# Kernel optimization log

Hardware: AMD Instinct MI355X
Metric: run time of the kernel (lower is better)

## Reference

```python
import jax, jax.numpy as jnp
from jax import lax
import numpy as np

B, T, IN, H = 8192, 512, 5, 32


def setup_inputs() -> dict:
    key = jax.random.key(0)
    ks = jax.random.split(key, 7)
    s_ih = 1.0 / np.sqrt(H)
    return {
        "x": jax.random.normal(ks[0], (B, T, IN), dtype=jnp.float32),
        "W_ih": jax.random.normal(ks[1], (4 * H, IN), dtype=jnp.float32) * s_ih,
        "W_hh": jax.random.normal(ks[2], (4 * H, H), dtype=jnp.float32) * s_ih,
        "b_ih": jax.random.normal(ks[3], (4 * H,), dtype=jnp.float32) * s_ih,
        "b_hh": jax.random.normal(ks[4], (4 * H,), dtype=jnp.float32) * s_ih,
        "W_fc": jax.random.normal(ks[5], (1, H), dtype=jnp.float32) * s_ih,
        "b_fc": jax.random.normal(ks[6], (1,), dtype=jnp.float32) * s_ih,
    }


def reference(x, W_ih, W_hh, b_ih, b_hh, W_fc, b_fc):
    # x: [B, T, IN]. Single-layer batch-first LSTM (PyTorch gate order i,f,g,o),
    # then linear head on the final timestep's hidden state.
    b = x.shape[0]
    h0 = jnp.zeros((b, H), x.dtype)
    c0 = jnp.zeros((b, H), x.dtype)
    # Precompute input projections for all timesteps in one GEMM: [T, B, 4H]
    x_t = jnp.swapaxes(x, 0, 1)  # [T, B, IN]
    x_proj = jnp.einsum("tbi,gi->tbg", x_t, W_ih) + b_ih + b_hh

    def step(carry, xp):
        h, c = carry
        gates = xp + h @ W_hh.T  # [B, 4H]
        i, f, g, o = jnp.split(gates, 4, axis=-1)
        i = jax.nn.sigmoid(i)
        f = jax.nn.sigmoid(f)
        g = jnp.tanh(g)
        o = jax.nn.sigmoid(o)
        c = f * c + i * g
        h = o * jnp.tanh(c)
        return (h, c), None

    (h_last, _), _ = lax.scan(step, (h0, c0), x_proj)
    return h_last @ W_fc.T + b_fc  # [B, 1]
```

## Files before the change

kernel.cpp:

```cpp
#include <hip/hip_runtime.h>


typedef __attribute__((ext_vector_type(8))) _Float16 half8;
typedef __attribute__((ext_vector_type(4))) float f32x4;
typedef __attribute__((ext_vector_type(4))) unsigned int u32x4;

static constexpr int BB  = 8192;
static constexpr int TT  = 512;
static constexpr int NIN = 5;
static constexpr int HH  = 32;

__device__ __forceinline__ unsigned short f16b(float f) {
    _Float16 h = (_Float16)f;
    return __builtin_bit_cast(unsigned short, h);
}
__device__ __forceinline__ float fast_sigmoid(float x) {
    float e = __builtin_amdgcn_exp2f(-1.4426950408889634f * x);
    return __builtin_amdgcn_rcpf(1.0f + e);
}
__device__ __forceinline__ float fast_tanh(float x) {
    float e = __builtin_amdgcn_exp2f(2.8853900817779268f * x);
    return 1.0f - 2.0f * __builtin_amdgcn_rcpf(1.0f + e);
}

__global__ __launch_bounds__(64) void lstm_f16(
    const float* __restrict__ x,
    const float* __restrict__ W_ih,
    const float* __restrict__ W_hh,
    const float* __restrict__ b_ih,
    const float* __restrict__ b_hh,
    const float* __restrict__ W_fc,
    const float* __restrict__ b_fc,
    float* __restrict__ out)
{
    const int lane = threadIdx.x & 63;
    const int col  = lane & 15;
    const int kg   = lane >> 4;
    const int b0   = blockIdx.x * 8;
    const int bloc = col & 7;
    const bool jlow = (col < 8);
    const int jbase = 4 * kg + (jlow ? 0 : 16);

    half8 Ahh[8], Ax[8];
#pragma unroll
    for (int t4 = 0; t4 < 8; ++t4) {
        const int gr = 16 * t4 + col;
#pragma unroll
        for (int e = 0; e < 8; ++e)
            Ahh[t4][e] = (_Float16)W_hh[gr * HH + kg * 8 + e];
        half8 v;
#pragma unroll
        for (int e = 0; e < 8; ++e) v[e] = (_Float16)0.f;
        if (kg == 0) {
#pragma unroll
            for (int e = 0; e < NIN; ++e) v[e] = (_Float16)W_ih[gr * NIN + e];
            float bias = b_ih[gr] + b_hh[gr];
            _Float16 bh_ = (_Float16)bias;
            v[5] = bh_;
            v[6] = (_Float16)(bias - (float)bh_);
        }
        Ax[t4] = v;
    }

    const int srcA = 32 * (kg & 1) + bloc + 8 * (kg >> 1);
    const int srcB = srcA + 16;

    const bool xk = (kg == 0);

    const float* px = x + (size_t)(b0 + bloc) * TT * NIN;
    float x0 = px[0], x1 = px[1], x2 = px[2], x3 = px[3], x4 = px[4];

    unsigned int bh0 = 0, bh1 = 0, bh2 = 0, bh3 = 0;
    float c0 = 0.f, c1 = 0.f, c2 = 0.f, c3 = 0.f;
    float h0 = 0.f, h1 = 0.f, h2 = 0.f, h3 = 0.f;
    const f32x4 z = {0.f, 0.f, 0.f, 0.f};

    auto make_bx = [&](float v0, float v1, float v2, float v3, float v4) -> half8 {
        unsigned w0 = (unsigned)f16b(v0) | ((unsigned)f16b(v1) << 16);
        unsigned w1 = (unsigned)f16b(v2) | ((unsigned)f16b(v3) << 16);
        unsigned w2 = (unsigned)f16b(v4) | (0x3C00u << 16);
        unsigned w3 = 0x00003C00u;
        u32x4 u = {xk ? w0 : 0u, xk ? w1 : 0u, xk ? w2 : 0u, xk ? w3 : 0u};
        return __builtin_bit_cast(half8, u);
    };

    f32x4 accN[8];
    {
        half8 bx0 = make_bx(x0, x1, x2, x3, x4);
#pragma unroll
        for (int t4 = 0; t4 < 8; ++t4)
            accN[t4] = __builtin_amdgcn_mfma_f32_16x16x32_f16(Ax[t4], bx0, z, 0, 0, 0);
    }

#pragma unroll 1
    for (int t = 0; t < TT; ++t) {
        const size_t off = (size_t)((t + 1 < TT) ? (t + 1) : t) * NIN;
        float n0 = px[off + 0], n1 = px[off + 1], n2 = px[off + 2],
              n3 = px[off + 3], n4 = px[off + 4];

        u32x4 bhu = {bh0, bh1, bh2, bh3};
        half8 bh = __builtin_bit_cast(half8, bhu);
        f32x4 acc[8];
#pragma unroll
        for (int t4 = 0; t4 < 8; ++t4)
            acc[t4] = __builtin_amdgcn_mfma_f32_16x16x32_f16(Ahh[t4], bh, accN[t4], 0, 0, 0);

        half8 bxn = make_bx(n0, n1, n2, n3, n4);
#pragma unroll
        for (int t4 = 0; t4 < 8; ++t4)
            accN[t4] = __builtin_amdgcn_mfma_f32_16x16x32_f16(Ax[t4], bxn, z, 0, 0, 0);

#pragma unroll
        for (int r = 0; r < 4; ++r) {
            float gi = jlow ? acc[0][r] : acc[1][r];
            float gf = jlow ? acc[2][r] : acc[3][r];
            float gg = jlow ? acc[4][r] : acc[5][r];
            float go = jlow ? acc[6][r] : acc[7][r];
            float iv = fast_sigmoid(gi);
            float fv = fast_sigmoid(gf);
            float gv = fast_tanh(gg);
            float ov = fast_sigmoid(go);
            float cc = (r == 0 ? c0 : r == 1 ? c1 : r == 2 ? c2 : c3);
            cc = fmaf(fv, cc, iv * gv);
            float hh = ov * fast_tanh(cc);
            if (r == 0) { c0 = cc; h0 = hh; }
            else if (r == 1) { c1 = cc; h1 = hh; }
            else if (r == 2) { c2 = cc; h2 = hh; }
            else { c3 = cc; h3 = hh; }
        }

        unsigned int p0 = (unsigned)f16b(h0) | ((unsigned)f16b(h1) << 16);
        unsigned int p1 = (unsigned)f16b(h2) | ((unsigned)f16b(h3) << 16);
        bh0 = (unsigned)__shfl((int)p0, srcA, 64);
        bh1 = (unsigned)__shfl((int)p1, srcA, 64);
        bh2 = (unsigned)__shfl((int)p0, srcB, 64);
        bh3 = (unsigned)__shfl((int)p1, srcB, 64);

        x0 = n0; x1 = n1; x2 = n2; x3 = n3; x4 = n4;
    }

    float v = h0 * W_fc[jbase + 0] + h1 * W_fc[jbase + 1]
            + h2 * W_fc[jbase + 2] + h3 * W_fc[jbase + 3];
    v += __shfl_xor(v, 8);
    v += __shfl_xor(v, 16);
    v += __shfl_xor(v, 32);
    if (lane < 8) out[b0 + lane] = v + b_fc[0];
}

extern "C" void kernel_launch(void* const* d_in, const int* in_sizes, int n_in,
                              void* d_out, int out_size, void* d_ws, size_t ws_size,
                              hipStream_t stream) {
    const float* x    = (const float*)d_in[0];
    const float* W_ih = (const float*)d_in[1];
    const float* W_hh = (const float*)d_in[2];
    const float* b_ih = (const float*)d_in[3];
    const float* b_hh = (const float*)d_in[4];
    const float* W_fc = (const float*)d_in[5];
    const float* b_fc = (const float*)d_in[6];
    float* out = (float*)d_out;

    lstm_f16<<<dim3(BB / 8), dim3(64), 0, stream>>>(
        x, W_ih, W_hh, b_ih, b_hh, W_fc, b_fc, out);
}
```

Before: 270.8 us.

## Split each 8-sequence block across two waves with 4 sequences per wave

Each wave now handles 4 batch rows instead of 8, so every lane computes 2 LSTM cells per step instead of 4, and the gate-element to lane mapping and shuffle sources are remapped to match. The launch uses 128-thread blocks with two waves each, doubling the wave count. The intent is to shorten the serial elementwise and transcendental part of each recurrent step and to give the scheduler more waves to hide MFMA and shuffle latency. In exchange, half of each MFMA's batch columns carry redundant work, so total MFMA issue doubles.

```diff
diff --git a/kernel.cpp b/kernel.cpp
--- a/kernel.cpp
+++ b/kernel.cpp
@@ -23,7 +23,7 @@
     return 1.0f - 2.0f * __builtin_amdgcn_rcpf(1.0f + e);
 }
 
-__global__ __launch_bounds__(64) void lstm_f16(
+__global__ __launch_bounds__(128) void lstm_f16x2(
     const float* __restrict__ x,
     const float* __restrict__ W_ih,
     const float* __restrict__ W_hh,
@@ -33,13 +33,17 @@
     const float* __restrict__ b_fc,
     float* __restrict__ out)
 {
-    const int lane = threadIdx.x & 63;
+    const int tid  = threadIdx.x;
+    const int w    = tid >> 6;
+    const int lane = tid & 63;
     const int col  = lane & 15;
     const int kg   = lane >> 4;
-    const int b0   = blockIdx.x * 8;
-    const int bloc = col & 7;
-    const bool jlow = (col < 8);
-    const int jbase = 4 * kg + (jlow ? 0 : 16);
+    const int bloc = col & 3;
+    const int q    = col >> 2;
+    const int jsel = q & 1;
+    const int rp   = q >> 1;
+    const int base = blockIdx.x * 8 + 4 * w;
+    const int j0   = 16 * jsel + 4 * kg + 2 * rp;
 
     half8 Ahh[8], Ax[8];
 #pragma unroll
@@ -62,17 +66,27 @@
         Ax[t4] = v;
     }
 
-    const int srcA = 32 * (kg & 1) + bloc + 8 * (kg >> 1);
-    const int srcB = srcA + 16;
+    int src0, src1, src2, src3;
+    {
+        int s[4];
+#pragma unroll
+        for (int m = 0; m < 4; ++m) {
+            const int J  = 8 * kg + 2 * m;
+            const int js = J >> 4;
+            const int kp = (J & 15) >> 2;
+            const int rq = (J >> 1) & 1;
+            s[m] = 16 * kp + 4 * (2 * rq + js) + bloc;
+        }
+        src0 = s[0]; src1 = s[1]; src2 = s[2]; src3 = s[3];
+    }
 
     const bool xk = (kg == 0);
 
-    const float* px = x + (size_t)(b0 + bloc) * TT * NIN;
+    const float* px = x + (size_t)(base + bloc) * TT * NIN;
     float x0 = px[0], x1 = px[1], x2 = px[2], x3 = px[3], x4 = px[4];
 
     unsigned int bh0 = 0, bh1 = 0, bh2 = 0, bh3 = 0;
-    float c0 = 0.f, c1 = 0.f, c2 = 0.f, c3 = 0.f;
-    float h0 = 0.f, h1 = 0.f, h2 = 0.f, h3 = 0.f;
+    float cc0 = 0.f, cc1 = 0.f, hh0 = 0.f, hh1 = 0.f;
     const f32x4 z = {0.f, 0.f, 0.f, 0.f};
 
     auto make_bx = [&](float v0, float v1, float v2, float v3, float v4) -> half8 {
@@ -110,41 +124,50 @@
         for (int t4 = 0; t4 < 8; ++t4)
             accN[t4] = __builtin_amdgcn_mfma_f32_16x16x32_f16(Ax[t4], bxn, z, 0, 0, 0);
 
+        float g0[4], g1[4];
 #pragma unroll
-        for (int r = 0; r < 4; ++r) {
-            float gi = jlow ? acc[0][r] : acc[1][r];
-            float gf = jlow ? acc[2][r] : acc[3][r];
-            float gg = jlow ? acc[4][r] : acc[5][r];
-            float go = jlow ? acc[6][r] : acc[7][r];
-            float iv = fast_sigmoid(gi);
-            float fv = fast_sigmoid(gf);
-            float gv = fast_tanh(gg);
-            float ov = fast_sigmoid(go);
-            float cc = (r == 0 ? c0 : r == 1 ? c1 : r == 2 ? c2 : c3);
-            cc = fmaf(fv, cc, iv * gv);
-            float hh = ov * fast_tanh(cc);
-            if (r == 0) { c0 = cc; h0 = hh; }
-            else if (r == 1) { c1 = cc; h1 = hh; }
-            else if (r == 2) { c2 = cc; h2 = hh; }
-            else { c3 = cc; h3 = hh; }
+        for (int G = 0; G < 4; ++G) {
+            const f32x4 tA = acc[2 * G], tB = acc[2 * G + 1];
+            float a0 = rp ? tA[2] : tA[0];
+            float a1 = rp ? tA[3] : tA[1];
+            float b0v = rp ? tB[2] : tB[0];
+            float b1v = rp ? tB[3] : tB[1];
+            g0[G] = jsel ? b0v : a0;
+            g1[G] = jsel ? b1v : a1;
         }
 
-        unsigned int p0 = (unsigned)f16b(h0) | ((unsigned)f16b(h1) << 16);
-        unsigned int p1 = (unsigned)f16b(h2) | ((unsigned)f16b(h3) << 16);
-        bh0 = (unsigned)__shfl((int)p0, srcA, 64);
-        bh1 = (unsigned)__shfl((int)p1, srcA, 64);
-        bh2 = (unsigned)__shfl((int)p0, srcB, 64);
-        bh3 = (unsigned)__shfl((int)p1, srcB, 64);
+        {
+            float iv = fast_sigmoid(g0[0]);
+            float fv = fast_sigmoid(g0[1]);
+            float gv = fast_tanh(g0[2]);
+            float ov = fast_sigmoid(g0[3]);
+            cc0 = fmaf(fv, cc0, iv * gv);
+            hh0 = ov * fast_tanh(cc0);
+        }
+        {
+            float iv = fast_sigmoid(g1[0]);
+            float fv = fast_sigmoid(g1[1]);
+            float gv = fast_tanh(g1[2]);
+            float ov = fast_sigmoid(g1[3]);
+            cc1 = fmaf(fv, cc1, iv * gv);
+            hh1 = ov * fast_tanh(cc1);
+        }
+
+        unsigned int p = (unsigned)f16b(hh0) | ((unsigned)f16b(hh1) << 16);
+        bh0 = (unsigned)__shfl((int)p, src0, 64);
+        bh1 = (unsigned)__shfl((int)p, src1, 64);
+        bh2 = (unsigned)__shfl((int)p, src2, 64);
+        bh3 = (unsigned)__shfl((int)p, src3, 64);
 
         x0 = n0; x1 = n1; x2 = n2; x3 = n3; x4 = n4;
     }
 
-    float v = h0 * W_fc[jbase + 0] + h1 * W_fc[jbase + 1]
-            + h2 * W_fc[jbase + 2] + h3 * W_fc[jbase + 3];
+    float v = hh0 * W_fc[j0] + hh1 * W_fc[j0 + 1];
+    v += __shfl_xor(v, 4);
     v += __shfl_xor(v, 8);
     v += __shfl_xor(v, 16);
     v += __shfl_xor(v, 32);
-    if (lane < 8) out[b0 + lane] = v + b_fc[0];
+    if (lane < 4) out[base + lane] = v + b_fc[0];
 }
 
 extern "C" void kernel_launch(void* const* d_in, const int* in_sizes, int n_in,
@@ -159,6 +182,6 @@
     const float* b_fc = (const float*)d_in[6];
     float* out = (float*)d_out;
 
-    lstm_f16<<<dim3(BB / 8), dim3(64), 0, stream>>>(
+    lstm_f16x2<<<dim3(BB / 8), dim3(128), 0, stream>>>(
         x, W_ih, W_hh, b_ih, b_hh, W_fc, b_fc, out);
 }
```

New measurement: 362.7 us. +33.9%, slower.

## Replace cross-lane shuffles with DPP row swap by permuting W_hh K layout

Applied to the files above, without the earlier changes.

Reorders the K dimension of the W_hh MFMA operand so each lane's own hidden outputs line up with the B-operand slots it needs, leaving only a swap between adjacent 8-lane halves. That swap uses a DPP row-shift in place of four ds_bpermute shuffles, taking LDS-latency permutes off the serial recurrence path. It also switches f16 packing to the cvt_pkrtz instruction, which rounds toward zero instead of to nearest and so changes numerics slightly.

```diff
diff --git a/kernel.cpp b/kernel.cpp
--- a/kernel.cpp
+++ b/kernel.cpp
@@ -10,9 +10,9 @@
 static constexpr int NIN = 5;
 static constexpr int HH  = 32;
 
-__device__ __forceinline__ unsigned short f16b(float f) {
-    _Float16 h = (_Float16)f;
-    return __builtin_bit_cast(unsigned short, h);
+__device__ __forceinline__ unsigned int pkrtz(float a, float b) {
+    auto h = __builtin_amdgcn_cvt_pkrtz(a, b);
+    return __builtin_bit_cast(unsigned int, h);
 }
 __device__ __forceinline__ float fast_sigmoid(float x) {
     float e = __builtin_amdgcn_exp2f(-1.4426950408889634f * x);
@@ -22,8 +22,11 @@
     float e = __builtin_amdgcn_exp2f(2.8853900817779268f * x);
     return 1.0f - 2.0f * __builtin_amdgcn_rcpf(1.0f + e);
 }
+__device__ __forceinline__ unsigned int xor8_dpp(unsigned int v) {
+    return (unsigned int)__builtin_amdgcn_mov_dpp((int)v, 0x128, 0xF, 0xF, false);
+}
 
-__global__ __launch_bounds__(64) void lstm_f16(
+__global__ __launch_bounds__(64) void lstm_dpp(
     const float* __restrict__ x,
     const float* __restrict__ W_ih,
     const float* __restrict__ W_hh,
@@ -46,8 +49,10 @@
     for (int t4 = 0; t4 < 8; ++t4) {
         const int gr = 16 * t4 + col;
 #pragma unroll
-        for (int e = 0; e < 8; ++e)
-            Ahh[t4][e] = (_Float16)W_hh[gr * HH + kg * 8 + e];
+        for (int e = 0; e < 8; ++e) {
+            const int sigma = (e < 4) ? (4 * kg + e) : (16 + 4 * kg + (e - 4));
+            Ahh[t4][e] = (_Float16)W_hh[gr * HH + sigma];
+        }
         half8 v;
 #pragma unroll
         for (int e = 0; e < 8; ++e) v[e] = (_Float16)0.f;
@@ -62,23 +67,20 @@
         Ax[t4] = v;
     }
 
-    const int srcA = 32 * (kg & 1) + bloc + 8 * (kg >> 1);
-    const int srcB = srcA + 16;
-
     const bool xk = (kg == 0);
 
     const float* px = x + (size_t)(b0 + bloc) * TT * NIN;
     float x0 = px[0], x1 = px[1], x2 = px[2], x3 = px[3], x4 = px[4];
 
-    unsigned int bh0 = 0, bh1 = 0, bh2 = 0, bh3 = 0;
     float c0 = 0.f, c1 = 0.f, c2 = 0.f, c3 = 0.f;
     float h0 = 0.f, h1 = 0.f, h2 = 0.f, h3 = 0.f;
+    unsigned int p0 = 0, p1 = 0;
     const f32x4 z = {0.f, 0.f, 0.f, 0.f};
 
     auto make_bx = [&](float v0, float v1, float v2, float v3, float v4) -> half8 {
-        unsigned w0 = (unsigned)f16b(v0) | ((unsigned)f16b(v1) << 16);
-        unsigned w1 = (unsigned)f16b(v2) | ((unsigned)f16b(v3) << 16);
-        unsigned w2 = (unsigned)f16b(v4) | (0x3C00u << 16);
+        unsigned w0 = pkrtz(v0, v1);
+        unsigned w1 = pkrtz(v2, v3);
+        unsigned w2 = pkrtz(v4, 1.0f);
         unsigned w3 = 0x00003C00u;
         u32x4 u = {xk ? w0 : 0u, xk ? w1 : 0u, xk ? w2 : 0u, xk ? w3 : 0u};
         return __builtin_bit_cast(half8, u);
@@ -98,8 +100,12 @@
         float n0 = px[off + 0], n1 = px[off + 1], n2 = px[off + 2],
               n3 = px[off + 3], n4 = px[off + 4];
 
-        u32x4 bhu = {bh0, bh1, bh2, bh3};
+        unsigned int q0 = xor8_dpp(p0);
+        unsigned int q1 = xor8_dpp(p1);
+        u32x4 bhu = {jlow ? p0 : q0, jlow ? p1 : q1,
+                     jlow ? q0 : p0, jlow ? q1 : p1};
         half8 bh = __builtin_bit_cast(half8, bhu);
+
         f32x4 acc[8];
 #pragma unroll
         for (int t4 = 0; t4 < 8; ++t4)
@@ -129,12 +135,8 @@
             else { c3 = cc; h3 = hh; }
         }
 
-        unsigned int p0 = (unsigned)f16b(h0) | ((unsigned)f16b(h1) << 16);
-        unsigned int p1 = (unsigned)f16b(h2) | ((unsigned)f16b(h3) << 16);
-        bh0 = (unsigned)__shfl((int)p0, srcA, 64);
-        bh1 = (unsigned)__shfl((int)p1, srcA, 64);
-        bh2 = (unsigned)__shfl((int)p0, srcB, 64);
-        bh3 = (unsigned)__shfl((int)p1, srcB, 64);
+        p0 = pkrtz(h0, h1);
+        p1 = pkrtz(h2, h3);
 
         x0 = n0; x1 = n1; x2 = n2; x3 = n3; x4 = n4;
     }
@@ -159,6 +161,6 @@
     const float* b_fc = (const float*)d_in[6];
     float* out = (float*)d_out;
 
-    lstm_f16<<<dim3(BB / 8), dim3(64), 0, stream>>>(
+    lstm_dpp<<<dim3(BB / 8), dim3(64), 0, stream>>>(
         x, W_ih, W_hh, b_ih, b_hh, W_fc, b_fc, out);
 }
```

Result: slower. 296.5 us (+9.5%).
